# Kernel optimization log

Hardware: AMD Instinct MI355X
Metric: run time of the kernel (lower is better)

## Reference

```python
import jax, jax.numpy as jnp
import numpy as np

NUM_CLASSES = 1203
NO_OBJECT = NUM_CLASSES - 1  # CONSTANTS.NO_OBJECT_LABEL
BZ, N = 64, 100


def _cxcywh_to_xyxy(b):
    cx, cy, w, h = b[..., 0], b[..., 1], b[..., 2], b[..., 3]
    return jnp.stack([cx - w / 2, cy - h / 2, cx + w / 2, cy + h / 2], axis=-1)


def _pairwise_iou_np(a, b):
    # a: [M,4] xyxy, b: [K,4] xyxy -> [M,K]
    area_a = (a[:, 2] - a[:, 0]) * (a[:, 3] - a[:, 1])
    area_b = (b[:, 2] - b[:, 0]) * (b[:, 3] - b[:, 1])
    lt = np.maximum(a[:, None, :2], b[None, :, :2])
    rb = np.minimum(a[:, None, 2:], b[None, :, 2:])
    wh = np.clip(rb - lt, 0.0, None)
    inter = wh[..., 0] * wh[..., 1]
    union = area_a[:, None] + area_b[None, :] - inter
    return inter / np.maximum(union, 1e-9)


def _lsa(cost):
    # Exact Hungarian (Jonker-Volgenant / e-maxx potentials), square cost [n,n].
    # Returns col_of_row: assigned column (target) for each row (prediction).
    n = cost.shape[0]
    INF = 1e18
    u = np.zeros(n + 1)
    v = np.zeros(n + 1)
    p = np.zeros(n + 1, dtype=np.int64)   # p[j] = row matched to column j (1-indexed)
    way = np.zeros(n + 1, dtype=np.int64)
    for i in range(1, n + 1):
        p[0] = i
        j0 = 0
        minv = np.full(n + 1, INF)
        used = np.zeros(n + 1, dtype=bool)
        while True:
            used[j0] = True
            i0 = p[j0]
            cur = cost[i0 - 1] - u[i0] - v[1:]
            unused = ~used[1:]
            improve = unused & (cur < minv[1:])
            minv[1:][improve] = cur[improve]
            way[1:][improve] = j0
            masked = np.where(unused, minv[1:], INF)
            j1 = int(np.argmin(masked)) + 1
            delta = masked[j1 - 1]
            u[p[used]] += delta
            v[used] -= delta
            minv[1:][unused] -= delta
            j0 = j1
            if p[j0] == 0:
                break
        while j0 != 0:
            j1 = way[j0]
            p[j0] = p[j1]
            j0 = j1
    col_of_row = np.zeros(n, dtype=np.int64)
    for j in range(1, n + 1):
        col_of_row[p[j] - 1] = j - 1
    return col_of_row


def _cxcywh_to_xyxy_np(b):
    cx, cy, w, h = b[..., 0], b[..., 1], b[..., 2], b[..., 3]
    return np.stack([cx - w / 2, cy - h / 2, cx + w / 2, cy + h / 2], axis=-1)


def _hungarian_match(labs, lab_preds, bbox, bbox_preds):
    # numpy matcher, mirrors HungarianMatcher.forward (no_grad).
    bz = labs.shape[0]
    # stable softmax over classes
    z = lab_preds - lab_preds.max(axis=-1, keepdims=True)
    e = np.exp(z)
    probs = e / e.sum(axis=-1, keepdims=True)  # [bz,N,C]
    gt_idx = np.zeros(labs.shape, dtype=np.int64)
    for b in range(bz):
        cost_class = -probs[b][:, labs[b]]                                   # [N,N]
        cost_bbox = np.abs(bbox_preds[b][:, None, :] - bbox[b][None, :, :]).sum(-1)
        iou = _pairwise_iou_np(_cxcywh_to_xyxy_np(bbox_preds[b]),
                               _cxcywh_to_xyxy_np(bbox[b]))
        C = cost_class + cost_bbox + (1.0 - iou)
        gt_idx[b] = _lsa(C.astype(np.float64))  # row_ind == arange(N) for square C
    return gt_idx


def _elementwise_iou(a, b):
    # a, b: [...,4] xyxy, paired IoU
    lt = jnp.maximum(a[..., :2], b[..., :2])
    rb = jnp.minimum(a[..., 2:], b[..., 2:])
    wh = jnp.clip(rb - lt, 0.0)
    inter = wh[..., 0] * wh[..., 1]
    area_a = (a[..., 2] - a[..., 0]) * (a[..., 3] - a[..., 1])
    area_b = (b[..., 2] - b[..., 0]) * (b[..., 3] - b[..., 1])
    union = area_a + area_b - inter
    return inter / jnp.maximum(union, 1e-9)


def _detr_loss(labs, lab_preds, bbox, bbox_preds, gt_idx):
    # Re-gather GT by matching (pred side is identity since row_ind=arange(N)).
    new_labs = jnp.take_along_axis(labs, gt_idx, axis=1)                  # [bz,N]
    new_bbox = jnp.take_along_axis(bbox, gt_idx[..., None], axis=1)      # [bz,N,4]
    probs = jax.nn.softmax(lab_preds, axis=-1)
    pred_cls = jnp.argmax(probs, axis=-1)
    mask = (new_labs != NO_OBJECT) & (new_labs == pred_cls)              # [bz,N]
    # classification term: mean over ALL bz*N entries of -p[gt_label]
    loss_label = -jnp.take_along_axis(probs, new_labs[..., None], axis=2).squeeze(-1)
    loss_label = loss_label.mean()
    cnt = mask.sum()
    # L1: torch's bbox[mask] flattens -> .sum(-1).mean() is a plain SUM of |diff|
    l1 = jnp.sum(jnp.abs(new_bbox - bbox_preds) * mask[..., None])
    # IoU loss: mean over masked boxes of (1 - iou)
    iou = _elementwise_iou(_cxcywh_to_xyxy(new_bbox), _cxcywh_to_xyxy(bbox_preds))
    liou = jnp.sum((1.0 - iou) * mask) / jnp.maximum(cnt, 1)
    return loss_label + l1 + liou


def setup_inputs() -> dict:
    key = jax.random.key(0)
    k1, k2, k3, k4 = jax.random.split(key, 4)
    labs = jax.random.randint(k1, (BZ, N), 0, NUM_CLASSES, dtype=jnp.int64)
    lab_preds = jax.random.normal(k2, (BZ, N, NUM_CLASSES), dtype=jnp.float32)
    bbox = jax.random.uniform(k3, (BZ, N, 4), dtype=jnp.float32)
    bbox_preds = jax.random.uniform(k4, (BZ, N, 4), dtype=jnp.float32)
    return {"labs": labs, "lab_preds": lab_preds, "bbox": bbox, "bbox_preds": bbox_preds}


def reference(labs, lab_preds, bbox, bbox_preds):
    gt_idx = _hungarian_match(np.asarray(labs),
                              np.asarray(lab_preds, dtype=np.float64),
                              np.asarray(bbox, dtype=np.float64),
                              np.asarray(bbox_preds, dtype=np.float64))
    return _detr_loss(labs, lab_preds, bbox, bbox_preds, jnp.asarray(gt_idx))
```

## Files before the change

kernel.cpp:

```cpp
#include <hip/hip_runtime.h>
#include <hip/hip_bf16.h>
#include <math.h>
#include <float.h>

#define BZ 64
#define NQ 100
#define NCLS 1203
#define NO_OBJ 1202
constexpr double HUNG_INF = 1e18;
#define KINF 0xC3ABC16D674EC800ull

__device__ inline double readlane_f64(double x, int l) {
  int lo = __builtin_amdgcn_readlane(__double2loint(x), l);
  int hi = __builtin_amdgcn_readlane(__double2hiint(x), l);
  return __hiloint2double(hi, lo);
}

template <int CTRL>
__device__ inline unsigned dpp_mov_u32(unsigned x) {
  return (unsigned)__builtin_amdgcn_update_dpp((int)x, (int)x, CTRL, 0xF, 0xF, false);
}
__device__ inline unsigned umin32(unsigned a, unsigned b) { return a < b ? a : b; }

__device__ inline unsigned wave_min_u32(unsigned x) {
  x = umin32(x, dpp_mov_u32<0xB1>(x));
  x = umin32(x, dpp_mov_u32<0x4E>(x));
  x = umin32(x, dpp_mov_u32<0x141>(x));
  x = umin32(x, dpp_mov_u32<0x128>(x));
  unsigned a = (unsigned)__builtin_amdgcn_readlane((int)x, 0);
  unsigned c = (unsigned)__builtin_amdgcn_readlane((int)x, 16);
  unsigned d = (unsigned)__builtin_amdgcn_readlane((int)x, 32);
  unsigned e = (unsigned)__builtin_amdgcn_readlane((int)x, 48);
  return umin32(umin32(a, c), umin32(d, e));
}

__device__ inline unsigned long long f64_key(double d) {
  long long b = __double_as_longlong(d);
  long long m = (b >> 63) | (long long)0x8000000000000000ll;
  return (unsigned long long)(b ^ m);
}
__device__ inline double key_to_f64(unsigned long long k) {
  long long kk = (long long)k;
  long long m = ((~kk) >> 63) | (long long)0x8000000000000000ll;
  return __longlong_as_double(kk ^ m);
}

__global__ __launch_bounds__(64) void rowstats_kernel(
    const float* __restrict__ lab_preds,
    double* __restrict__ rowmax, double* __restrict__ rowsum,
    float* __restrict__ mxf, float* __restrict__ sf, int* __restrict__ amx) {
  const int r = blockIdx.x;
  const int t = threadIdx.x;
  const float* row = lab_preds + (size_t)r * NCLS;
  float fm = -FLT_MAX; int am = NCLS;
  for (int c = t; c < NCLS; c += 64) {
    float vv = row[c];
    if (vv > fm) { fm = vv; am = c; }
  }
#pragma unroll
  for (int off = 32; off; off >>= 1) {
    float ov = __shfl_xor(fm, off); int oi = __shfl_xor(am, off);
    if (ov > fm || (ov == fm && oi < am)) { fm = ov; am = oi; }
  }
  const double mx = (double)fm;
  double s = 0.0;
  for (int c = t; c < NCLS; c += 64) s += exp((double)row[c] - mx);
#pragma unroll
  for (int off = 32; off; off >>= 1) s += __shfl_xor(s, off);
  float sfl = 0.0f;
  for (int c = t; c < NCLS; c += 64) sfl += expf(row[c] - fm);
#pragma unroll
  for (int off = 32; off; off >>= 1) sfl += __shfl_xor(sfl, off);
  if (t == 0) {
    rowmax[r] = mx; rowsum[r] = s;
    mxf[r] = fm; sf[r] = sfl; amx[r] = am;
  }
}

__global__ __launch_bounds__(64) void match_kernel(
    const int* __restrict__ labs, const float* __restrict__ lab_preds,
    const float* __restrict__ bbox, const float* __restrict__ bbox_preds,
    const double* __restrict__ rowmax, const double* __restrict__ rowsum,
    int* __restrict__ gt_idx) {
  __shared__ double2 Csh2[NQ * 64];
  __shared__ int labs_sh[NQ];
  __shared__ double pxy[NQ][4], txy[NQ][4], pcx[NQ][4], tcx[NQ][4];
  __shared__ double areaP[NQ], areaT[NQ], rmax[NQ], rsum[NQ];

  const int b = blockIdx.x;
  const int lane = threadIdx.x;

  for (int j = lane; j < NQ; j += 64) {
    labs_sh[j] = labs[b * NQ + j];
    const float* tb = bbox + ((size_t)b * NQ + j) * 4;
    double cx = tb[0], cy = tb[1], w = tb[2], h = tb[3];
    tcx[j][0] = cx; tcx[j][1] = cy; tcx[j][2] = w; tcx[j][3] = h;
    double x1 = cx - w * 0.5, y1 = cy - h * 0.5, x2 = cx + w * 0.5, y2 = cy + h * 0.5;
    txy[j][0] = x1; txy[j][1] = y1; txy[j][2] = x2; txy[j][3] = y2;
    areaT[j] = (x2 - x1) * (y2 - y1);
    const float* pb = bbox_preds + ((size_t)b * NQ + j) * 4;
    cx = pb[0]; cy = pb[1]; w = pb[2]; h = pb[3];
    pcx[j][0] = cx; pcx[j][1] = cy; pcx[j][2] = w; pcx[j][3] = h;
    x1 = cx - w * 0.5; y1 = cy - h * 0.5; x2 = cx + w * 0.5; y2 = cy + h * 0.5;
    pxy[j][0] = x1; pxy[j][1] = y1; pxy[j][2] = x2; pxy[j][3] = y2;
    areaP[j] = (x2 - x1) * (y2 - y1);
    rmax[j] = rowmax[b * NQ + j];
    rsum[j] = rowsum[b * NQ + j];
  }
  __syncthreads();

  for (int i = 0; i < NQ; ++i) {
    double cA, cB = 0.0;
    {
      const int j = lane;
      double pc = exp((double)lab_preds[((size_t)b * NQ + i) * NCLS + labs_sh[j]] - rmax[i]) / rsum[i];
      double cb = fabs(pcx[i][0] - tcx[j][0]) + fabs(pcx[i][1] - tcx[j][1])
                + fabs(pcx[i][2] - tcx[j][2]) + fabs(pcx[i][3] - tcx[j][3]);
      double ltx = fmax(pxy[i][0], txy[j][0]);
      double lty = fmax(pxy[i][1], txy[j][1]);
      double rbx = fmin(pxy[i][2], txy[j][2]);
      double rby = fmin(pxy[i][3], txy[j][3]);
      double inter = fmax(rbx - ltx, 0.0) * fmax(rby - lty, 0.0);
      double uni = areaP[i] + areaT[j] - inter;
      double iou = inter / fmax(uni, 1e-9);
      cA = -pc + cb + (1.0 - iou);
    }
    if (lane + 64 < NQ) {
      const int j = lane + 64;
      double pc = exp((double)lab_preds[((size_t)b * NQ + i) * NCLS + labs_sh[j]] - rmax[i]) / rsum[i];
      double cb = fabs(pcx[i][0] - tcx[j][0]) + fabs(pcx[i][1] - tcx[j][1])
                + fabs(pcx[i][2] - tcx[j][2]) + fabs(pcx[i][3] - tcx[j][3]);
      double ltx = fmax(pxy[i][0], txy[j][0]);
      double lty = fmax(pxy[i][1], txy[j][1]);
      double rbx = fmin(pxy[i][2], txy[j][2]);
      double rby = fmin(pxy[i][3], txy[j][3]);
      double inter = fmax(rbx - ltx, 0.0) * fmax(rby - lty, 0.0);
      double uni = areaP[i] + areaT[j] - inter;
      double iou = inter / fmax(uni, 1e-9);
      cB = -pc + cb + (1.0 - iou);
    }
    Csh2[i * 64 + lane] = make_double2(cA, cB);
  }
  __syncthreads();

  const bool has1 = (lane + 65 <= NQ);
  double v0 = 0.0, v1 = 0.0;
  double u0 = 0.0, u1 = 0.0;
  int p0c = 0, p1c = 0;

  for (int i = 1; i <= NQ; ++i) {
    double minv0 = HUNG_INF, minv1 = HUNG_INF;
    int way0 = 0, way1 = 0;
    bool used0 = false, used1 = false;
    double u_i = 0.0;
    int j0 = 0, i0 = i;
    double ui0 = 0.0;
    double2 cd = Csh2[(i0 - 1) * 64 + lane];
    while (true) {
      if (j0 == lane + 1) used0 = true;
      if (j0 == lane + 65) used1 = true;

      const double c0 = cd.x;
      const double c1 = cd.y;

      if (!used0) {
        double cur = (c0 - ui0) - v0;
        if (cur < minv0) { minv0 = cur; way0 = j0; }
      }
      if (has1 && !used1) {
        double cur = (c1 - ui0) - v1;
        if (cur < minv1) { minv1 = cur; way1 = j0; }
      }
      const unsigned long long k0 = used0 ? KINF : f64_key(minv0);
      const unsigned long long k1 = has1 ? (used1 ? KINF : f64_key(minv1)) : ~0ull;

      const unsigned h0 = (unsigned)(k0 >> 32), h1 = (unsigned)(k1 >> 32);
      const unsigned KH = wave_min_u32(umin32(h0, h1));
      unsigned long long blh0 = __ballot(h0 == KH);
      unsigned long long blh1 = __ballot(h1 == KH);
      int j1, lj;
      unsigned long long KEY;
      if (__popcll(blh0) + __popcll(blh1) == 1) {
        if (blh0) {
          lj = (int)__ffsll(blh0) - 1; j1 = lj + 1;
          KEY = ((unsigned long long)KH << 32) |
                (unsigned)__builtin_amdgcn_readlane((int)(unsigned)k0, lj);
        } else {
          lj = (int)__ffsll(blh1) - 1; j1 = lj + 65;
          KEY = ((unsigned long long)KH << 32) |
                (unsigned)__builtin_amdgcn_readlane((int)(unsigned)k1, lj);
        }
      } else {
        const unsigned lo0 = (h0 == KH) ? (unsigned)k0 : 0xFFFFFFFFu;
        const unsigned lo1 = (h1 == KH) ? (unsigned)k1 : 0xFFFFFFFFu;
        const unsigned KL = wave_min_u32(umin32(lo0, lo1));
        KEY = ((unsigned long long)KH << 32) | KL;
        unsigned long long bl0 = __ballot(k0 == KEY);
        if (bl0) { lj = (int)__ffsll(bl0) - 1; j1 = lj + 1; }
        else {
          unsigned long long bl1 = __ballot(k1 == KEY);
          lj = (int)__ffsll(bl1) - 1; j1 = lj + 65;
        }
      }

      int pj1; double uj1;
      if (j1 <= 64) { pj1 = __builtin_amdgcn_readlane(p0c, lj); uj1 = readlane_f64(u0, lj); }
      else          { pj1 = __builtin_amdgcn_readlane(p1c, lj); uj1 = readlane_f64(u1, lj); }
      const int nrow = (pj1 > 0 ? pj1 : 1) - 1;
      double2 cd_next = Csh2[nrow * 64 + lane];

      const double delta = key_to_f64(KEY);
      if (used0)        { v0 -= delta; u0 += delta; }
      else              { minv0 -= delta; }
      if (has1) {
        if (used1)      { v1 -= delta; u1 += delta; }
        else            { minv1 -= delta; }
      }
      u_i += delta;

      j0 = j1; i0 = pj1; ui0 = uj1; cd = cd_next;
      if (pj1 == 0) break;
    }
    int jj = j0;
    while (jj != 0) {
      int ljj = (jj <= 64) ? (jj - 1) : (jj - 65);
      int jn = (jj <= 64) ? __builtin_amdgcn_readlane(way0, ljj)
                          : __builtin_amdgcn_readlane(way1, ljj);
      int pn; double un;
      if (jn == 0) { pn = i; un = u_i; }
      else {
        int ln = (jn <= 64) ? (jn - 1) : (jn - 65);
        if (jn <= 64) { pn = __builtin_amdgcn_readlane(p0c, ln); un = readlane_f64(u0, ln); }
        else          { pn = __builtin_amdgcn_readlane(p1c, ln); un = readlane_f64(u1, ln); }
      }
      if (jj == lane + 1)  { p0c = pn; u0 = un; }
      if (jj == lane + 65) { p1c = pn; u1 = un; }
      jj = jn;
    }
  }

  gt_idx[b * NQ + p0c - 1] = lane;
  if (has1) gt_idx[b * NQ + p1c - 1] = lane + 64;
}

__global__ __launch_bounds__(256) void lossfinal_kernel(
    const int* __restrict__ labs, const float* __restrict__ lab_preds,
    const float* __restrict__ bbox, const float* __restrict__ bbox_preds,
    const int* __restrict__ gt_idx,
    const float* __restrict__ mxf, const float* __restrict__ sf,
    const int* __restrict__ amx,
    double* __restrict__ acc, int* __restrict__ cnt_out) {
  const int r = blockIdx.x * 256 + threadIdx.x;
  double lab_t = 0.0, l1_t = 0.0, iou_t = 0.0;
  int c_t = 0;
  if (r < BZ * NQ) {
    const int b = r / NQ;
    const int g = gt_idx[r];
    const int nl = labs[b * NQ + g];
    const float val = lab_preds[(size_t)r * NCLS + nl];
    const float pg = expf(val - mxf[r]) / sf[r];
    lab_t = -(double)pg;
    if (nl != NO_OBJ && nl == amx[r]) {
      c_t = 1;
      const float* pb = bbox_preds + (size_t)r * 4;
      const float* tb = bbox + ((size_t)b * NQ + g) * 4;
      float l1 = fabsf(tb[0] - pb[0]) + fabsf(tb[1] - pb[1])
               + fabsf(tb[2] - pb[2]) + fabsf(tb[3] - pb[3]);
      l1_t = (double)l1;
      float px1 = pb[0] - pb[2] * 0.5f, py1 = pb[1] - pb[3] * 0.5f;
      float px2 = pb[0] + pb[2] * 0.5f, py2 = pb[1] + pb[3] * 0.5f;
      float tx1 = tb[0] - tb[2] * 0.5f, ty1 = tb[1] - tb[3] * 0.5f;
      float tx2 = tb[0] + tb[2] * 0.5f, ty2 = tb[1] + tb[3] * 0.5f;
      float ltx = fmaxf(px1, tx1), lty = fmaxf(py1, ty1);
      float rbx = fminf(px2, tx2), rby = fminf(py2, ty2);
      float inter = fmaxf(rbx - ltx, 0.0f) * fmaxf(rby - lty, 0.0f);
      float uni = (px2 - px1) * (py2 - py1) + (tx2 - tx1) * (ty2 - ty1) - inter;
      float iou = inter / fmaxf(uni, 1e-9f);
      iou_t = (double)(1.0f - iou);
    }
  }
#pragma unroll
  for (int off = 32; off; off >>= 1) {
    lab_t += __shfl_xor(lab_t, off);
    l1_t  += __shfl_xor(l1_t, off);
    iou_t += __shfl_xor(iou_t, off);
    c_t   += __shfl_xor(c_t, off);
  }
  __shared__ double s_lab[4], s_l1[4], s_iou[4];
  __shared__ int s_cnt[4];
  const int wave = threadIdx.x >> 6;
  if ((threadIdx.x & 63) == 0) { s_lab[wave] = lab_t; s_l1[wave] = l1_t; s_iou[wave] = iou_t; s_cnt[wave] = c_t; }
  __syncthreads();
  if (threadIdx.x == 0) {
    double a = 0.0, bb = 0.0, c = 0.0; int n = 0;
    for (int w = 0; w < 4; ++w) { a += s_lab[w]; bb += s_l1[w]; c += s_iou[w]; n += s_cnt[w]; }
    atomicAdd(&acc[0], a);
    atomicAdd(&acc[1], bb);
    atomicAdd(&acc[2], c);
    atomicAdd(cnt_out, n);
  }
}

__global__ void finalize_kernel(const double* __restrict__ acc, const int* __restrict__ cnt,
                                float* __restrict__ out) {
  int n = *cnt; if (n < 1) n = 1;
  out[0] = (float)(acc[0] / (double)(BZ * NQ) + acc[1] + acc[2] / (double)n);
}

extern "C" void kernel_launch(void* const* d_in, const int* in_sizes, int n_in,
                              void* d_out, int out_size, void* d_ws, size_t ws_size,
                              hipStream_t stream) {
  const int*   labs       = (const int*)d_in[0];
  const float* lab_preds  = (const float*)d_in[1];
  const float* bbox       = (const float*)d_in[2];
  const float* bbox_preds = (const float*)d_in[3];

  char* ws = (char*)d_ws;
  int*    gt_idx = (int*)ws;
  double* acc    = (double*)(ws + 25600);
  int*    cnt    = (int*)(ws + 25624);
  double* rowmax = (double*)(ws + 25632);
  double* rowsum = (double*)(ws + 76832);
  float*  mxf    = (float*)(ws + 128032);
  float*  sfw    = (float*)(ws + 153632);
  int*    amx    = (int*)(ws + 179232);

  hipMemsetAsync(ws + 25600, 0, 32, stream);
  rowstats_kernel<<<BZ * NQ, 64, 0, stream>>>(lab_preds, rowmax, rowsum, mxf, sfw, amx);
  match_kernel<<<BZ, 64, 0, stream>>>(labs, lab_preds, bbox, bbox_preds, rowmax, rowsum, gt_idx);
  lossfinal_kernel<<<(BZ * NQ + 255) / 256, 256, 0, stream>>>(
      labs, lab_preds, bbox, bbox_preds, gt_idx, mxf, sfw, amx, acc, cnt);
  finalize_kernel<<<1, 1, 0, stream>>>(acc, cnt, (float*)d_out);
}
```

Before: 555.5 us.

## Warm-start Hungarian with column reduction and auction-style augmenting row transfer

Adds a Jonker-Volgenant style initialization before the Hungarian loop: column minima set the initial dual potentials v, columns greedily claim their argmin row through shared-memory CAS, and a bounded augmenting-row-transfer pass (up to 400 iterations) assigns further free rows using wave-wide two-smallest reductions. Only rows still free afterwards go through the full shortest-augmenting-path search. This is meant to cut the number of costly sequential Dijkstra-like iterations per batch, at the cost of extra setup work and the risk that the result differs from the reference on ties.

```diff
diff --git a/kernel.cpp b/kernel.cpp
--- a/kernel.cpp
+++ b/kernel.cpp
@@ -21,6 +21,9 @@
   return (unsigned)__builtin_amdgcn_update_dpp((int)x, (int)x, CTRL, 0xF, 0xF, false);
 }
 __device__ inline unsigned umin32(unsigned a, unsigned b) { return a < b ? a : b; }
+__device__ inline unsigned long long umin64(unsigned long long a, unsigned long long b) {
+  return a < b ? a : b;
+}
 
 __device__ inline unsigned wave_min_u32(unsigned x) {
   x = umin32(x, dpp_mov_u32<0xB1>(x));
@@ -32,6 +35,14 @@
   unsigned d = (unsigned)__builtin_amdgcn_readlane((int)x, 32);
   unsigned e = (unsigned)__builtin_amdgcn_readlane((int)x, 48);
   return umin32(umin32(a, c), umin32(d, e));
+}
+
+__device__ inline unsigned long long wave_min_u64(unsigned long long k) {
+  unsigned h = (unsigned)(k >> 32);
+  unsigned KH = wave_min_u32(h);
+  unsigned lo = (h == KH) ? (unsigned)k : 0xFFFFFFFFu;
+  unsigned KL = wave_min_u32(lo);
+  return ((unsigned long long)KH << 32) | KL;
 }
 
 __device__ inline unsigned long long f64_key(double d) {
@@ -84,6 +95,7 @@
     int* __restrict__ gt_idx) {
   __shared__ double2 Csh2[NQ * 64];
   __shared__ int labs_sh[NQ];
+  __shared__ int rowclaim[NQ];
   __shared__ double pxy[NQ][4], txy[NQ][4], pcx[NQ][4], tcx[NQ][4];
   __shared__ double areaP[NQ], areaT[NQ], rmax[NQ], rsum[NQ];
 
@@ -107,6 +119,7 @@
     rmax[j] = rowmax[b * NQ + j];
     rsum[j] = rowsum[b * NQ + j];
   }
+  for (int r = lane; r < NQ; r += 64) rowclaim[r] = -1;
   __syncthreads();
 
   for (int i = 0; i < NQ; ++i) {
@@ -144,16 +157,74 @@
   __syncthreads();
 
   const bool has1 = (lane + 65 <= NQ);
-  double v0 = 0.0, v1 = 0.0;
+
+  double mn0 = DBL_MAX, mn1 = DBL_MAX; int ar0 = 0, ar1 = 0;
+  for (int i = 0; i < NQ; ++i) {
+    double2 cd = Csh2[i * 64 + lane];
+    if (cd.x < mn0) { mn0 = cd.x; ar0 = i; }
+    if (has1 && cd.y < mn1) { mn1 = cd.y; ar1 = i; }
+  }
+  double v0 = mn0, v1 = has1 ? mn1 : 0.0;
   double u0 = 0.0, u1 = 0.0;
   int p0c = 0, p1c = 0;
-
-  for (int i = 1; i <= NQ; ++i) {
+  if (atomicCAS(&rowclaim[ar0], -1, lane) == -1) p0c = ar0 + 1;
+  if (has1 && atomicCAS(&rowclaim[ar1], -1, 64 + lane) == -1) p1c = ar1 + 1;
+  __syncthreads();
+
+  int cl0 = rowclaim[lane];
+  unsigned long long fm0 = __ballot(cl0 == -1);
+  int cl1 = (lane < NQ - 64) ? rowclaim[64 + lane] : 0;
+  unsigned long long fm1 = __ballot((lane < NQ - 64) && cl1 == -1);
+
+  int budget = 400;
+  while ((fm0 | fm1) && budget-- > 0) {
+    int f = fm0 ? ((int)__ffsll(fm0) - 1) : (64 + (int)__ffsll(fm1) - 1);
+    double2 cf = Csh2[f * 64 + lane];
+    double r0 = cf.x - v0;
+    double r1 = cf.y - v1;
+    unsigned long long k0 = f64_key(r0);
+    unsigned long long k1 = has1 ? f64_key(r1) : ~0ull;
+    unsigned long long K1 = wave_min_u64(umin64(k0, k1));
+    unsigned long long bl0 = __ballot(k0 == K1);
+    int lj, slot;
+    if (bl0) { lj = (int)__ffsll(bl0) - 1; slot = 0; }
+    else { unsigned long long bl1 = __ballot(k1 == K1); lj = (int)__ffsll(bl1) - 1; slot = 1; }
+    unsigned long long k0b = (slot == 0 && lane == lj) ? ~0ull : k0;
+    unsigned long long k1b = (slot == 1 && lane == lj) ? ~0ull : k1;
+    unsigned long long K2 = wave_min_u64(umin64(k0b, k1b));
+    double m1 = key_to_f64(K1), m2 = key_to_f64(K2);
+    int i1 = (slot == 0) ? __builtin_amdgcn_readlane(p0c, lj)
+                         : __builtin_amdgcn_readlane(p1c, lj);
+    const bool own0 = (slot == 0 && lane == lj);
+    const bool own1 = (slot == 1 && lane == lj);
+    if (i1 == 0) {
+      if (own0) { p0c = f + 1; u0 = m1; }
+      if (own1) { p1c = f + 1; u1 = m1; }
+    } else {
+      if (m1 < m2) {
+        if (own0) { v0 -= (m2 - m1); p0c = f + 1; u0 = m2; }
+        if (own1) { v1 -= (m2 - m1); p1c = f + 1; u1 = m2; }
+      } else {
+        if (own0) { p0c = f + 1; u0 = m1; }
+        if (own1) { p1c = f + 1; u1 = m1; }
+      }
+      int k = i1 - 1;
+      if (k < 64) fm0 |= (1ull << k); else fm1 |= (1ull << (k - 64));
+    }
+    if (f < 64) fm0 &= ~(1ull << f); else fm1 &= ~(1ull << (f - 64));
+  }
+
+  while (fm0 | fm1) {
+    int f;
+    if (fm0) { f = (int)__ffsll(fm0) - 1; fm0 &= fm0 - 1; }
+    else     { f = 64 + (int)__ffsll(fm1) - 1; fm1 &= fm1 - 1; }
+    const int fi = f + 1;
+
     double minv0 = HUNG_INF, minv1 = HUNG_INF;
     int way0 = 0, way1 = 0;
     bool used0 = false, used1 = false;
     double u_i = 0.0;
-    int j0 = 0, i0 = i;
+    int j0 = 0, i0 = fi;
     double ui0 = 0.0;
     double2 cd = Csh2[(i0 - 1) * 64 + lane];
     while (true) {
@@ -227,7 +298,7 @@
       int jn = (jj <= 64) ? __builtin_amdgcn_readlane(way0, ljj)
                           : __builtin_amdgcn_readlane(way1, ljj);
       int pn; double un;
-      if (jn == 0) { pn = i; un = u_i; }
+      if (jn == 0) { pn = fi; un = u_i; }
       else {
         int ln = (jn <= 64) ? (jn - 1) : (jn - 65);
         if (jn <= 64) { pn = __builtin_amdgcn_readlane(p0c, ln); un = readlane_f64(u0, ln); }
```

Result: slower. 639.7 us (+15.1%).
